# Kernel tuning notes

Measured on AMD Instinct MI355X. Metric: run time of the kernel, lower is better.

Reference implementation:

```python
import jax, jax.numpy as jnp
import numpy as np

NHID = 1024
NHEAD = 16
HEAD_DIM = 64
B, L = 8, 4096

def setup_inputs() -> dict:
    key = jax.random.key(0)
    ks = jax.random.split(key, 12)
    s_in = 1.0 / np.sqrt(NHID)
    s_o = 1.0 / np.sqrt(NHEAD * HEAD_DIM)
    return {
        'x': jax.random.normal(ks[0], (B, L, NHID), dtype=jnp.float32),
        'ax': jax.random.normal(ks[1], (B, NHID), dtype=jnp.float32),
        'WQ_w': jax.random.normal(ks[2], (NHID, NHEAD * HEAD_DIM), dtype=jnp.float32) * s_in,
        'WQ_b': jnp.zeros((NHEAD * HEAD_DIM,), dtype=jnp.float32),
        'WK_w': jax.random.normal(ks[3], (NHID, NHEAD * HEAD_DIM), dtype=jnp.float32) * s_in,
        'WK_b': jnp.zeros((NHEAD * HEAD_DIM,), dtype=jnp.float32),
        'WV_w': jax.random.normal(ks[4], (NHID, NHEAD * HEAD_DIM), dtype=jnp.float32) * s_in,
        'WV_b': jnp.zeros((NHEAD * HEAD_DIM,), dtype=jnp.float32),
        'WO_w': jax.random.normal(ks[5], (NHEAD * HEAD_DIM, NHID), dtype=jnp.float32) * s_o,
        'WO_b': jnp.zeros((NHID,), dtype=jnp.float32),
    }

def reference(x, ax, WQ_w, WQ_b, WK_w, WK_b, WV_w, WV_b, WO_w, WO_b):
    Bx, Lx, H = x.shape
    nh, d = NHEAD, HEAD_DIM
    q = (x @ WQ_w + WQ_b).reshape(Bx, Lx, nh, d)
    k = (x @ WK_w + WK_b).reshape(Bx, Lx, nh, d)
    # global token projections (note: source's v local slots use K due to pad_v=F.pad(k,...) bug)
    ak = (ax @ WK_w + WK_b).reshape(Bx, 1, nh, d)
    av = (ax @ WV_w + WV_b).reshape(Bx, 1, nh, d)
    # shifted local window (unfold_size=3), pad seq dim by 1 on each side
    pad_k = jnp.pad(k, ((0, 0), (1, 1), (0, 0), (0, 0)))  # (B, L+2, nh, d)
    k_shift = jnp.stack([pad_k[:, t:Lx + t] for t in range(3)], axis=3)  # (B,L,nh,3,d)
    akb = jnp.broadcast_to(ak, (Bx, Lx, nh, d))[:, :, :, None, :]  # (B,L,nh,1,d)
    avb = jnp.broadcast_to(av, (Bx, Lx, nh, d))[:, :, :, None, :]
    K = jnp.concatenate([akb, k_shift], axis=3)  # (B,L,nh,4,d)
    V = jnp.concatenate([avb, k_shift], axis=3)  # local V slots = K (faithful to source bug)
    scores = jnp.einsum('blhd,blhjd->blhj', q, K) / jnp.sqrt(jnp.float32(d))
    alphas = jax.nn.softmax(scores, axis=-1)  # dropout = identity (eval)
    att = jnp.einsum('blhj,blhjd->blhd', alphas, V).reshape(Bx, Lx, nh * d)
    return att @ WO_w + WO_b
```

## Files before the change

### kernel.cpp

```cpp
#include <hip/hip_runtime.h>
#include <hip/hip_bf16.h>

typedef __bf16 bf16x8 __attribute__((ext_vector_type(8)));
typedef __bf16 bf16x4 __attribute__((ext_vector_type(4)));
typedef float  floatx4 __attribute__((ext_vector_type(4)));

#define L_SEQ 4096

__global__ void cvt_bf16_kernel(const float* __restrict__ src,
                                __bf16* __restrict__ dst, int n8)
{
    int i = blockIdx.x * blockDim.x + threadIdx.x;
    if (i >= n8) return;
    const float4* s = (const float4*)src + (size_t)i * 2;
    float4 f0 = s[0], f1 = s[1];
    bf16x8 o;
    o[0] = (__bf16)f0.x; o[1] = (__bf16)f0.y; o[2] = (__bf16)f0.z; o[3] = (__bf16)f0.w;
    o[4] = (__bf16)f1.x; o[5] = (__bf16)f1.y; o[6] = (__bf16)f1.z; o[7] = (__bf16)f1.w;
    *((bf16x8*)dst + i) = o;
}

__global__ void transpose_cvt3_kernel(const float* __restrict__ WQ,
                                      const float* __restrict__ WK,
                                      const float* __restrict__ WO,
                                      __bf16* __restrict__ Wqk,
                                      __bf16* __restrict__ Wo)
{
    const int z = blockIdx.z;
    const float* src = (z == 0) ? WQ : (z == 1) ? WK : WO;
    __bf16* dst = (z == 0) ? Wqk : (z == 1) ? (Wqk + (size_t)1024 * 1024) : Wo;

    __shared__ float tile[32][33];
    int tx = threadIdx.x & 31, ty = threadIdx.x >> 5;
    int n0 = blockIdx.x * 32, k0 = blockIdx.y * 32;
    #pragma unroll
    for (int i = 0; i < 32; i += 8)
        tile[ty + i][tx] = src[(size_t)(k0 + ty + i) * 1024 + n0 + tx];
    __syncthreads();
    #pragma unroll
    for (int i = 0; i < 32; i += 8)
        dst[(size_t)(n0 + ty + i) * 1024 + k0 + tx] = (__bf16)tile[tx][ty + i];
}

__global__ void akv_part_kernel(const float* __restrict__ ax,
                                const float* __restrict__ Wk,
                                const float* __restrict__ Wv,
                                float* __restrict__ part)
{
    int b = blockIdx.x, kv = blockIdx.y, z = blockIdx.z;
    int n = threadIdx.x * 4;
    const float* W   = kv ? Wv : Wk;
    const float* axr = ax + (size_t)b * 1024 + z * 128;
    float4 acc = {0.f, 0.f, 0.f, 0.f};
    for (int k = 0; k < 128; ++k) {
        float a = axr[k];
        float4 w = *(const float4*)(W + (size_t)(z * 128 + k) * 1024 + n);
        acc.x = fmaf(a, w.x, acc.x);
        acc.y = fmaf(a, w.y, acc.y);
        acc.z = fmaf(a, w.z, acc.z);
        acc.w = fmaf(a, w.w, acc.w);
    }
    *(float4*)(part + (((size_t)(b * 2 + kv)) * 8 + z) * 1024 + n) = acc;
}

__global__ void akv_reduce_kernel(const float* __restrict__ part,
                                  const float* __restrict__ bk,
                                  const float* __restrict__ bv,
                                  float* __restrict__ akv)
{
    int b = blockIdx.x, kv = blockIdx.y;
    int n = threadIdx.x * 4;
    float4 acc = *(const float4*)((kv ? bv : bk) + n);
    #pragma unroll
    for (int z = 0; z < 8; ++z) {
        float4 p = *(const float4*)(part + (((size_t)(b * 2 + kv)) * 8 + z) * 1024 + n);
        acc.x += p.x; acc.y += p.y; acc.z += p.z; acc.w += p.w;
    }
    *(float4*)(akv + ((size_t)b * 2 + kv) * 1024 + n) = acc;
}

template <int NPX, bool OUT_F32>
__global__ __launch_bounds__(256, 4) void gemm_bt_kernel(
    const __bf16* __restrict__ A, const __bf16* __restrict__ Bt,
    const float* __restrict__ b0, const float* __restrict__ b1, int nsplit,
    void* __restrict__ Cp, int M, int N, int K)
{
    __shared__ __bf16 As[128 * 32];
    __shared__ __bf16 Bs[128 * 32];
    const int bid  = blockIdx.x;
    const int xcd  = bid & 7, g = bid >> 3;
    const int nt   = xcd * NPX + (g % NPX);
    const int mt   = g / NPX;
    const int m0 = mt * 128, n0 = nt * 128;

    const int tid  = threadIdx.x;
    const int wave = tid >> 6, lane = tid & 63;
    const int quad = lane >> 4, l16 = lane & 15;
    const int wm = (wave >> 1) * 64, wn = (wave & 1) * 64;

    floatx4 acc[4][4] = {};

    const int srow  = lane >> 2;
    const int skcol = (lane & 3) * 8;

    for (int k0 = 0; k0 < K; k0 += 32) {
        if (k0) __syncthreads();
        #pragma unroll
        for (int c = 0; c < 2; ++c) {
            int chunk = wave * 2 + c;
            int row   = chunk * 16 + srow;
            __builtin_amdgcn_global_load_lds(
                (const __attribute__((address_space(1))) void*)(A + (size_t)(m0 + row) * K + k0 + skcol),
                (__attribute__((address_space(3))) void*)(As + chunk * 512),
                16, 0, 0);
            __builtin_amdgcn_global_load_lds(
                (const __attribute__((address_space(1))) void*)(Bt + (size_t)(n0 + row) * K + k0 + skcol),
                (__attribute__((address_space(3))) void*)(Bs + chunk * 512),
                16, 0, 0);
        }
        __syncthreads();

        bf16x8 af[4], bfr[4];
        #pragma unroll
        for (int mi = 0; mi < 4; ++mi)
            af[mi] = *(const bf16x8*)(As + (wm + mi * 16 + l16) * 32 + quad * 8);
        #pragma unroll
        for (int ni = 0; ni < 4; ++ni)
            bfr[ni] = *(const bf16x8*)(Bs + (wn + ni * 16 + l16) * 32 + quad * 8);
        #pragma unroll
        for (int mi = 0; mi < 4; ++mi)
            #pragma unroll
            for (int ni = 0; ni < 4; ++ni)
                acc[mi][ni] = __builtin_amdgcn_mfma_f32_16x16x32_bf16(
                    af[mi], bfr[ni], acc[mi][ni], 0, 0, 0);
    }

    #pragma unroll
    for (int ni = 0; ni < 4; ++ni) {
        int gn = n0 + wn + ni * 16 + l16;
        float bv = (gn < nsplit) ? b0[gn] : b1[gn - nsplit];
        #pragma unroll
        for (int mi = 0; mi < 4; ++mi) {
            int gm = m0 + wm + mi * 16 + quad * 4;
            #pragma unroll
            for (int r = 0; r < 4; ++r) {
                float v = acc[mi][ni][r] + bv;
                if (OUT_F32)
                    ((float*)Cp)[(size_t)(gm + r) * N + gn] = v;
                else
                    ((__bf16*)Cp)[(size_t)(gm + r) * N + gn] = (__bf16)v;
            }
        }
    }
}

__global__ void attn_kernel(const __bf16* __restrict__ qk,
                            const float* __restrict__ akv,
                            __bf16* __restrict__ att)
{
    const int t  = threadIdx.x;
    const int c4 = t * 4;
    const int m0 = blockIdx.x * 8;
    const int l0 = m0 & (L_SEQ - 1);
    const int b  = m0 >> 12;

    float kr[10][4];
    #pragma unroll
    for (int j = 0; j < 10; ++j) {
        int ll = l0 - 1 + j;
        if (ll >= 0 && ll < L_SEQ) {
            bf16x4 kv = *(const bf16x4*)(qk + (size_t)(m0 - 1 + j) * 2048 + 1024 + c4);
            kr[j][0] = kv[0]; kr[j][1] = kv[1]; kr[j][2] = kv[2]; kr[j][3] = kv[3];
        } else {
            kr[j][0] = kr[j][1] = kr[j][2] = kr[j][3] = 0.f;
        }
    }
    float4 ak4 = *(const float4*)(akv + ((size_t)b * 2 + 0) * 1024 + c4);
    float4 av4 = *(const float4*)(akv + ((size_t)b * 2 + 1) * 1024 + c4);

    #pragma unroll
    for (int i = 0; i < 8; ++i) {
        const int m = m0 + i;
        bf16x4 qv = *(const bf16x4*)(qk + (size_t)m * 2048 + c4);
        float q0 = qv[0], q1 = qv[1], q2 = qv[2], q3 = qv[3];

        float p0 = q0 * ak4.x + q1 * ak4.y + q2 * ak4.z + q3 * ak4.w;
        float p1 = q0 * kr[i][0]     + q1 * kr[i][1]     + q2 * kr[i][2]     + q3 * kr[i][3];
        float p2 = q0 * kr[i + 1][0] + q1 * kr[i + 1][1] + q2 * kr[i + 1][2] + q3 * kr[i + 1][3];
        float p3 = q0 * kr[i + 2][0] + q1 * kr[i + 2][1] + q2 * kr[i + 2][2] + q3 * kr[i + 2][3];
        #pragma unroll
        for (int off = 1; off < 16; off <<= 1) {
            p0 += __shfl_xor(p0, off, 64);
            p1 += __shfl_xor(p1, off, 64);
            p2 += __shfl_xor(p2, off, 64);
            p3 += __shfl_xor(p3, off, 64);
        }
        const float sc = 0.125f;
        float s0 = p0 * sc, s1 = p1 * sc, s2 = p2 * sc, s3 = p3 * sc;
        float mx = fmaxf(fmaxf(s0, s1), fmaxf(s2, s3));
        float e0 = __expf(s0 - mx), e1 = __expf(s1 - mx), e2 = __expf(s2 - mx), e3 = __expf(s3 - mx);
        float inv = 1.f / (e0 + e1 + e2 + e3);

        bf16x4 o;
        o[0] = (__bf16)((e0 * av4.x + e1 * kr[i][0] + e2 * kr[i + 1][0] + e3 * kr[i + 2][0]) * inv);
        o[1] = (__bf16)((e0 * av4.y + e1 * kr[i][1] + e2 * kr[i + 1][1] + e3 * kr[i + 2][1]) * inv);
        o[2] = (__bf16)((e0 * av4.z + e1 * kr[i][2] + e2 * kr[i + 1][2] + e3 * kr[i + 2][2]) * inv);
        o[3] = (__bf16)((e0 * av4.w + e1 * kr[i][3] + e2 * kr[i + 1][3] + e3 * kr[i + 2][3]) * inv);
        *(bf16x4*)(att + (size_t)m * 1024 + c4) = o;
    }
}

extern "C" void kernel_launch(void* const* d_in, const int* in_sizes, int n_in,
                              void* d_out, int out_size, void* d_ws, size_t ws_size,
                              hipStream_t stream)
{
    const float* x    = (const float*)d_in[0];
    const float* ax   = (const float*)d_in[1];
    const float* WQ_w = (const float*)d_in[2];
    const float* WQ_b = (const float*)d_in[3];
    const float* WK_w = (const float*)d_in[4];
    const float* WK_b = (const float*)d_in[5];
    const float* WV_w = (const float*)d_in[6];
    const float* WV_b = (const float*)d_in[7];
    const float* WO_w = (const float*)d_in[8];
    const float* WO_b = (const float*)d_in[9];
    float* out = (float*)d_out;

    const int M = 8 * 4096;

    char* ws = (char*)d_ws;
    __bf16* xb   = (__bf16*)(ws);
    __bf16* Wqk  = (__bf16*)(ws + 67108864);
    __bf16* Wo   = (__bf16*)(ws + 71303168);
    __bf16* qk   = (__bf16*)(ws + 73400320);
    __bf16* att  = (__bf16*)(ws + 207618048);
    float*  akv  = (float*)(ws + 274726912);
    float*  akvp = (float*)(ws + 274792448);

    {
        int n8 = (M * 1024) / 8;
        cvt_bf16_kernel<<<n8 / 256, 256, 0, stream>>>(x, xb, n8);
    }
    transpose_cvt3_kernel<<<dim3(32, 32, 3), 256, 0, stream>>>(WQ_w, WK_w, WO_w, Wqk, Wo);
    akv_part_kernel<<<dim3(8, 2, 8), 256, 0, stream>>>(ax, WK_w, WV_w, akvp);
    akv_reduce_kernel<<<dim3(8, 2), 256, 0, stream>>>(akvp, WK_b, WV_b, akv);
    gemm_bt_kernel<2, false><<<(M / 128) * 16, 256, 0, stream>>>(
        xb, Wqk, WQ_b, WK_b, 1024, (void*)qk, M, 2048, 1024);
    attn_kernel<<<M / 8, 256, 0, stream>>>(qk, akv, att);
    gemm_bt_kernel<1, true><<<(M / 128) * 8, 256, 0, stream>>>(
        att, Wo, WO_b, WO_b, 1024, (void*)out, M, 1024, 1024);
}
```

Before: 560.9 us.

## Replace 128x128 GEMM with 256x256 double-buffered, swizzled, ping-pong scheduled GEMM

Swaps the simple 128x128 single-buffer BF16 GEMM for a 256x256 tile kernel with 512 threads and 128 KB of LDS. It double-buffers K-tiles of 64, uses an XOR swizzle in LDS to avoid bank conflicts, and splits each iteration into four MFMA phases. Global-to-LDS loads for future tiles are interleaved between phases, with barriers and s_setprio controlling the order. Larger tiles raise data reuse and overlap loads with compute, but occupancy drops to one block per CU and the block-to-XCD mapping changes.

```diff
diff --git a/kernel.cpp b/kernel.cpp
--- a/kernel.cpp
+++ b/kernel.cpp
@@ -79,73 +79,158 @@
     *(float4*)(akv + ((size_t)b * 2 + kv) * 1024 + n) = acc;
 }
 
-template <int NPX, bool OUT_F32>
-__global__ __launch_bounds__(256, 4) void gemm_bt_kernel(
+#define GLDS(gp, lp) __builtin_amdgcn_global_load_lds(                              \
+    (const __attribute__((address_space(1))) void*)(gp),                            \
+    (__attribute__((address_space(3))) void*)(lp), 16, 0, 0)
+
+#define STAGE_A(hi, kt, buf) do {                                                   \
+    GLDS(A + aS[0][hi] + (size_t)(kt) * 64, smem + (buf) * 65536 + aD[0][hi]);      \
+    GLDS(A + aS[1][hi] + (size_t)(kt) * 64, smem + (buf) * 65536 + aD[1][hi]);      \
+} while (0)
+#define STAGE_B(hi, kt, buf) do {                                                   \
+    GLDS(Bt + bS[0][hi] + (size_t)(kt) * 64, smem + (buf) * 65536 + bD[0][hi]);     \
+    GLDS(Bt + bS[1][hi] + (size_t)(kt) * 64, smem + (buf) * 65536 + bD[1][hi]);     \
+} while (0)
+
+#define RDA(cb, mi, kk) (*(const bf16x8*)(smem + (cb) + awoff + ((mi) << 11) + ((kk) << 10)))
+#define RDB(cb, ni, kk) (*(const bf16x8*)(smem + (cb) + bwoff + ((ni) << 11) + ((kk) << 10)))
+#define MFMA16(af, bfv, c) (c) = __builtin_amdgcn_mfma_f32_16x16x32_bf16((af), (bfv), (c), 0, 0, 0)
+
+template <int NT, bool OUT_F32>
+__global__ __launch_bounds__(512, 2) void gemm256_kernel(
     const __bf16* __restrict__ A, const __bf16* __restrict__ Bt,
     const float* __restrict__ b0, const float* __restrict__ b1, int nsplit,
     void* __restrict__ Cp, int M, int N, int K)
 {
-    __shared__ __bf16 As[128 * 32];
-    __shared__ __bf16 Bs[128 * 32];
-    const int bid  = blockIdx.x;
-    const int xcd  = bid & 7, g = bid >> 3;
-    const int nt   = xcd * NPX + (g % NPX);
-    const int mt   = g / NPX;
-    const int m0 = mt * 128, n0 = nt * 128;
+    __shared__ __align__(16) char smem[131072];
+
+    const int bid = blockIdx.x;
+    const int xcd = bid & 7, g = bid >> 3;
+    int mt, nt;
+    if constexpr (NT == 8) { nt = xcd;     mt = g; }
+    else                   { nt = xcd & 3; mt = (xcd >> 2) * ((M >> 8) >> 1) + g; }
+    const int m0 = mt << 8, n0 = nt << 8;
 
     const int tid  = threadIdx.x;
     const int wave = tid >> 6, lane = tid & 63;
-    const int quad = lane >> 4, l16 = lane & 15;
-    const int wm = (wave >> 1) * 64, wn = (wave & 1) * 64;
-
-    floatx4 acc[4][4] = {};
-
-    const int srow  = lane >> 2;
-    const int skcol = (lane & 3) * 8;
-
-    for (int k0 = 0; k0 < K; k0 += 32) {
-        if (k0) __syncthreads();
+    const int l15  = lane & 15, quad = lane >> 4;
+    const int ntile = K >> 6;
+
+    const int rowin = lane >> 2;
+    const int colel = ((lane & 3) << 3) ^ (((lane >> 5) & 1) << 4);
+    size_t aS[2][2], bS[2][2];
+    int    aD[2][2], bD[2][2];
+    #pragma unroll
+    for (int hi = 0; hi < 2; ++hi) {
+        const int rgA = (wave & 3) + ((wave >> 2) << 3) + hi * 4;
+        const int rgB = ((wave >> 1) << 2) + (wave & 1) + hi * 2;
         #pragma unroll
         for (int c = 0; c < 2; ++c) {
-            int chunk = wave * 2 + c;
-            int row   = chunk * 16 + srow;
-            __builtin_amdgcn_global_load_lds(
-                (const __attribute__((address_space(1))) void*)(A + (size_t)(m0 + row) * K + k0 + skcol),
-                (__attribute__((address_space(3))) void*)(As + chunk * 512),
-                16, 0, 0);
-            __builtin_amdgcn_global_load_lds(
-                (const __attribute__((address_space(1))) void*)(Bt + (size_t)(n0 + row) * K + k0 + skcol),
-                (__attribute__((address_space(3))) void*)(Bs + chunk * 512),
-                16, 0, 0);
-        }
-        __syncthreads();
-
-        bf16x8 af[4], bfr[4];
+            aS[c][hi] = (size_t)(m0 + rgA * 16 + rowin) * K + c * 32 + colel;
+            aD[c][hi] = (rgA * 2 + c) << 10;
+            bS[c][hi] = (size_t)(n0 + rgB * 16 + rowin) * K + c * 32 + colel;
+            bD[c][hi] = 32768 + ((rgB * 2 + c) << 10);
+        }
+    }
+
+    const int alane = (l15 << 6) + ((quad << 4) ^ (((l15 >> 3) & 1) << 5));
+    const int awoff = (((wave >> 2) * 8) << 11) + alane;
+    const int bwoff = 32768 + (((wave & 3) * 4) << 11) + alane;
+
+    floatx4 acc[8][4] = {};
+
+    STAGE_A(0, 0, 0); STAGE_A(1, 0, 0); STAGE_B(0, 0, 0); STAGE_B(1, 0, 0);
+    STAGE_A(0, 1, 1); STAGE_B(0, 1, 1); STAGE_B(1, 1, 1);
+    asm volatile("s_waitcnt vmcnt(6)" ::: "memory");
+    __builtin_amdgcn_s_barrier();
+
+    for (int t = 0; t < ntile; ++t) {
+        const int p  = t & 1;
+        const int cb = p * 65536;
+        bf16x8 a0[4][2], a1[4][2], b0f[2][2], b1f[2][2];
+
+        #pragma unroll
+        for (int mi = 0; mi < 4; ++mi) { a0[mi][0] = RDA(cb, mi, 0); a0[mi][1] = RDA(cb, mi, 1); }
+        #pragma unroll
+        for (int ni = 0; ni < 2; ++ni) { b0f[ni][0] = RDB(cb, ni, 0); b0f[ni][1] = RDB(cb, ni, 1); }
+        if (t + 1 < ntile) STAGE_A(1, t + 1, p ^ 1);
+        __builtin_amdgcn_s_barrier();
+        asm volatile("s_waitcnt lgkmcnt(0)" ::: "memory");
+        __builtin_amdgcn_s_setprio(1);
         #pragma unroll
         for (int mi = 0; mi < 4; ++mi)
-            af[mi] = *(const bf16x8*)(As + (wm + mi * 16 + l16) * 32 + quad * 8);
-        #pragma unroll
-        for (int ni = 0; ni < 4; ++ni)
-            bfr[ni] = *(const bf16x8*)(Bs + (wn + ni * 16 + l16) * 32 + quad * 8);
+            #pragma unroll
+            for (int ni = 0; ni < 2; ++ni) {
+                MFMA16(a0[mi][0], b0f[ni][0], acc[mi][ni]);
+                MFMA16(a0[mi][1], b0f[ni][1], acc[mi][ni]);
+            }
+        __builtin_amdgcn_s_setprio(0);
+        __builtin_amdgcn_s_barrier();
+
+        #pragma unroll
+        for (int ni = 0; ni < 2; ++ni) { b1f[ni][0] = RDB(cb, ni + 2, 0); b1f[ni][1] = RDB(cb, ni + 2, 1); }
+        if (t + 2 < ntile) STAGE_A(0, t + 2, p);
+        __builtin_amdgcn_s_barrier();
+        asm volatile("s_waitcnt lgkmcnt(0)" ::: "memory");
+        __builtin_amdgcn_s_setprio(1);
         #pragma unroll
         for (int mi = 0; mi < 4; ++mi)
             #pragma unroll
-            for (int ni = 0; ni < 4; ++ni)
-                acc[mi][ni] = __builtin_amdgcn_mfma_f32_16x16x32_bf16(
-                    af[mi], bfr[ni], acc[mi][ni], 0, 0, 0);
-    }
-
+            for (int ni = 0; ni < 2; ++ni) {
+                MFMA16(a0[mi][0], b1f[ni][0], acc[mi][ni + 2]);
+                MFMA16(a0[mi][1], b1f[ni][1], acc[mi][ni + 2]);
+            }
+        __builtin_amdgcn_s_setprio(0);
+        __builtin_amdgcn_s_barrier();
+
+        #pragma unroll
+        for (int mi = 0; mi < 4; ++mi) { a1[mi][0] = RDA(cb, mi + 4, 0); a1[mi][1] = RDA(cb, mi + 4, 1); }
+        if (t + 2 < ntile) STAGE_B(0, t + 2, p);
+        __builtin_amdgcn_s_barrier();
+        asm volatile("s_waitcnt lgkmcnt(0)" ::: "memory");
+        __builtin_amdgcn_s_setprio(1);
+        #pragma unroll
+        for (int mi = 0; mi < 4; ++mi)
+            #pragma unroll
+            for (int ni = 0; ni < 2; ++ni) {
+                MFMA16(a1[mi][0], b1f[ni][0], acc[mi + 4][ni + 2]);
+                MFMA16(a1[mi][1], b1f[ni][1], acc[mi + 4][ni + 2]);
+            }
+        __builtin_amdgcn_s_setprio(0);
+        __builtin_amdgcn_s_barrier();
+
+        if (t + 2 < ntile) {
+            STAGE_B(1, t + 2, p);
+            asm volatile("s_waitcnt vmcnt(6)" ::: "memory");
+        } else {
+            asm volatile("s_waitcnt vmcnt(0)" ::: "memory");
+        }
+        __builtin_amdgcn_s_barrier();
+        __builtin_amdgcn_s_setprio(1);
+        #pragma unroll
+        for (int mi = 0; mi < 4; ++mi)
+            #pragma unroll
+            for (int ni = 0; ni < 2; ++ni) {
+                MFMA16(a1[mi][0], b0f[ni][0], acc[mi + 4][ni]);
+                MFMA16(a1[mi][1], b0f[ni][1], acc[mi + 4][ni]);
+            }
+        __builtin_amdgcn_s_setprio(0);
+        __builtin_amdgcn_s_barrier();
+    }
+
+    const int gmw = m0 + (wave >> 2) * 128;
+    const int gnw = n0 + (wave & 3) * 64;
     #pragma unroll
     for (int ni = 0; ni < 4; ++ni) {
-        int gn = n0 + wn + ni * 16 + l16;
+        int gn = gnw + ni * 16 + l15;
         float bv = (gn < nsplit) ? b0[gn] : b1[gn - nsplit];
         #pragma unroll
-        for (int mi = 0; mi < 4; ++mi) {
-            int gm = m0 + wm + mi * 16 + quad * 4;
+        for (int mi = 0; mi < 8; ++mi) {
+            int gm = gmw + mi * 16 + quad * 4;
             #pragma unroll
             for (int r = 0; r < 4; ++r) {
                 float v = acc[mi][ni][r] + bv;
-                if (OUT_F32)
+                if constexpr (OUT_F32)
                     ((float*)Cp)[(size_t)(gm + r) * N + gn] = v;
                 else
                     ((__bf16*)Cp)[(size_t)(gm + r) * N + gn] = (__bf16)v;
@@ -244,9 +329,9 @@
     transpose_cvt3_kernel<<<dim3(32, 32, 3), 256, 0, stream>>>(WQ_w, WK_w, WO_w, Wqk, Wo);
     akv_part_kernel<<<dim3(8, 2, 8), 256, 0, stream>>>(ax, WK_w, WV_w, akvp);
     akv_reduce_kernel<<<dim3(8, 2), 256, 0, stream>>>(akvp, WK_b, WV_b, akv);
-    gemm_bt_kernel<2, false><<<(M / 128) * 16, 256, 0, stream>>>(
+    gemm256_kernel<8, false><<<(M / 256) * 8, 512, 0, stream>>>(
         xb, Wqk, WQ_b, WK_b, 1024, (void*)qk, M, 2048, 1024);
     attn_kernel<<<M / 8, 256, 0, stream>>>(qk, akv, att);
-    gemm_bt_kernel<1, true><<<(M / 128) * 8, 256, 0, stream>>>(
+    gemm256_kernel<4, true><<<(M / 256) * 4, 512, 0, stream>>>(
         att, Wo, WO_b, WO_b, 1024, (void*)out, M, 1024, 1024);
 }
```

After: 549.8 us. -2.0%, faster.
